# Optimization experiments

Measured on AMD Instinct MI355X. Metric: run time of the kernel, lower is better.

Reference implementation:

```python
import jax, jax.numpy as jnp
import numpy as np

N_NODES = 50000
N_EDGES = 200000
D = 384
R = 2  # num_relations


def setup_inputs() -> dict:
    key = jax.random.key(0)
    ks = jax.random.split(key, 16)
    inp = {
        "embeddings": jax.random.normal(ks[0], (N_NODES, D), dtype=jnp.float32),
        "edge_index": jax.random.randint(ks[1], (2, N_EDGES), 0, N_NODES, dtype=jnp.int64),
        "edge_type": jax.random.randint(ks[2], (N_EDGES,), 0, R, dtype=jnp.int64),
    }
    # RGCNConv params for 3 layers: per-relation weight, root weight, bias
    s = 1.0 / np.sqrt(D)
    for i, kk in zip((1, 2, 3), range(3)):
        inp[f"W{i}"] = jax.random.uniform(ks[3 + 3 * kk], (R, D, D), dtype=jnp.float32, minval=-s, maxval=s)
        inp[f"root{i}"] = jax.random.uniform(ks[4 + 3 * kk], (D, D), dtype=jnp.float32, minval=-s, maxval=s)
        inp[f"bias{i}"] = jnp.zeros((D,), dtype=jnp.float32)
    return inp


def _rgcn_conv(x, src, dst, edge_type, W, root, bias):
    # PyG RGCNConv with aggr='mean': for each relation, mean-aggregate neighbor
    # features over edges of that relation, then apply relation weight; plus
    # root transform and bias. We transform-then-aggregate (equivalent, linear).
    out = x @ root + bias
    for r in range(R):
        xr = x @ W[r]                                   # [N, D]
        mask = (edge_type == r).astype(x.dtype)         # [E]
        msg = xr[src] * mask[:, None]                   # [E, D] gather
        s = jax.ops.segment_sum(msg, dst, num_segments=N_NODES)    # [N, D]
        cnt = jax.ops.segment_sum(mask, dst, num_segments=N_NODES)  # [N]
        out = out + s / jnp.maximum(cnt, 1.0)[:, None]  # mean (0 if no edges)
    return out


def reference(embeddings, edge_index, edge_type, W1, root1, bias1, W2, root2, bias2, W3, root3, bias3):
    src, dst = edge_index[0], edge_index[1]
    x = jax.nn.relu(_rgcn_conv(embeddings, src, dst, edge_type, W1, root1, bias1))
    # dropout is identity in eval mode
    x = jax.nn.relu(_rgcn_conv(x, src, dst, edge_type, W2, root2, bias2))
    x = _rgcn_conv(x, src, dst, edge_type, W3, root3, bias3)
    return x
```

## Files before the change

### kernel.cpp

```cpp
#include <hip/hip_runtime.h>
#include <hip/hip_bf16.h>


#define D 384
#define KC 1152
#define BM 128
#define BN 128
#define BK 32
#define NKT (KC / BK)
#define NTN (D / BN)

typedef __attribute__((ext_vector_type(8))) short short8;
typedef __attribute__((ext_vector_type(4))) float floatx4;
typedef unsigned int uint;
typedef unsigned short ushort;

#define BAR() asm volatile("s_barrier" ::: "memory")
#define WAIT_VM4() asm volatile("s_waitcnt vmcnt(4)" ::: "memory")
#define WAIT_VM0() asm volatile("s_waitcnt vmcnt(0)" ::: "memory")

__device__ __forceinline__ void load_lds16(const void* g, void* l) {
    __builtin_amdgcn_global_load_lds(
        (const __attribute__((address_space(1))) void*)g,
        (__attribute__((address_space(3))) void*)l, 16, 0, 0);
}

__device__ __forceinline__ ushort f2bf(float x) {
    __hip_bfloat16 h = __float2bfloat16(x);
    return *reinterpret_cast<ushort*>(&h);
}

__device__ __forceinline__ uint pack2(float a, float b) {
    return (uint)f2bf(a) | ((uint)f2bf(b) << 16);
}

__device__ __forceinline__ float bflo(uint u) { return __uint_as_float(u << 16); }
__device__ __forceinline__ float bfhi(uint u) { return __uint_as_float(u & 0xffff0000u); }

__device__ __forceinline__ void stage_rows(const ushort* __restrict__ g,
                                           size_t stride, int koff,
                                           ushort* l, int grow0, int rmax,
                                           int tid)
{
#pragma unroll
    for (int j = 0; j < 2; ++j) {
        const int ch = j * 256 + tid;
        const int row = ch >> 2;
        const int cs = ch & 3;
        const int gc = cs ^ ((row >> 1) & 3);
        const int gr = min(grow0 + row, rmax);
        load_lds16(g + (size_t)gr * stride + koff + gc * 8, l + (size_t)ch * 8);
    }
}

__global__ __launch_bounds__(256, 3) void gemm_fused(
    const ushort* __restrict__ X, const ushort* __restrict__ AG,
    const ushort* __restrict__ BT, const float* __restrict__ bias,
    ushort* __restrict__ Xn, float* __restrict__ outf,
    int M, int nwg, int relu)
{
    __shared__ alignas(16) ushort As[3][BM * BK];
    __shared__ alignas(16) ushort Bs[3][BN * BK];

    const int o = blockIdx.x;
    const int xcd = o & 7, lid = o >> 3;
    const int q = nwg >> 3, r = nwg & 7;
    const int wg = (xcd < r ? xcd * (q + 1) : r * (q + 1) + (xcd - r) * q) + lid;
    const int bnt = wg % NTN, bmt = wg / NTN;
    const int bm = bmt * BM, bn = bnt * BN;

    const int tid = threadIdx.x;
    const int wave = tid >> 6, lane = tid & 63;
    const int wm = wave >> 1;
    const int wn = wave & 1;
    const int l15 = lane & 15, k8 = lane >> 4;

    floatx4 acc[4][4] = {};

    auto stage_a = [&](int kt, ushort* dst) {
        if (kt < 12) stage_rows(X, 384, kt * BK, dst, bm, M - 1, tid);
        else         stage_rows(AG, 768, (kt - 12) * BK, dst, bm, M - 1, tid);
    };

    stage_a(0, As[0]);
    stage_rows(BT, KC, 0, Bs[0], bn, D - 1, tid);
    stage_a(1, As[1]);
    stage_rows(BT, KC, BK, Bs[1], bn, D - 1, tid);
    WAIT_VM4();
    BAR();

    for (int j = 0; j < NKT; ++j) {
        const ushort* Ab = As[j % 3];
        const ushort* Bb = Bs[j % 3];

        short8 af[4], bf[4];
#pragma unroll
        for (int nf = 0; nf < 4; ++nf) {
            const int rr = wn * 64 + nf * 16 + l15;
            af[nf] = *(const short8*)(Bb + rr * BK + ((k8 ^ ((rr >> 1) & 3)) << 3));
        }
#pragma unroll
        for (int mf = 0; mf < 4; ++mf) {
            const int rr = wm * 64 + mf * 16 + l15;
            bf[mf] = *(const short8*)(Ab + rr * BK + ((k8 ^ ((rr >> 1) & 3)) << 3));
        }

        const int js = j + 2;
        if (js < NKT) {
            stage_a(js, As[js % 3]);
            stage_rows(BT, KC, js * BK, Bs[js % 3], bn, D - 1, tid);
        }

        __builtin_amdgcn_s_setprio(1);
#pragma unroll
        for (int nf = 0; nf < 4; ++nf)
#pragma unroll
            for (int mf = 0; mf < 4; ++mf)
                acc[nf][mf] = __builtin_amdgcn_mfma_f32_16x16x32_bf16(
                    af[nf], bf[mf], acc[nf][mf], 0, 0, 0);
        __builtin_amdgcn_s_setprio(0);

        if (j <= NKT - 3)      { WAIT_VM4(); }
        else if (j == NKT - 2) { WAIT_VM0(); }
        BAR();
    }

    const int node0 = bm + wm * 64 + l15;
    const int colg = bn + wn * 64 + k8 * 4;
    float4 bv[4];
#pragma unroll
    for (int nf = 0; nf < 4; ++nf)
        bv[nf] = *(const float4*)(bias + colg + nf * 16);

#pragma unroll
    for (int mf = 0; mf < 4; ++mf) {
        const int node = node0 + mf * 16;
        if (node < M) {
            float v[4][4];
#pragma unroll
            for (int nf = 0; nf < 4; ++nf) {
                v[nf][0] = acc[nf][mf][0] + bv[nf].x;
                v[nf][1] = acc[nf][mf][1] + bv[nf].y;
                v[nf][2] = acc[nf][mf][2] + bv[nf].z;
                v[nf][3] = acc[nf][mf][3] + bv[nf].w;
                if (relu) {
#pragma unroll
                    for (int t = 0; t < 4; ++t) v[nf][t] = fmaxf(v[nf][t], 0.f);
                }
            }
            if (Xn) {
                uint2* rowp = (uint2*)(Xn + (size_t)node * D + colg);
#pragma unroll
                for (int nf = 0; nf < 4; ++nf) {
                    uint2 o2;
                    o2.x = pack2(v[nf][0], v[nf][1]);
                    o2.y = pack2(v[nf][2], v[nf][3]);
                    rowp[nf * 4] = o2;
                }
            } else {
                float4* rowp = (float4*)(outf + (size_t)node * D + colg);
#pragma unroll
                for (int nf = 0; nf < 4; ++nf)
                    rowp[nf * 4] = make_float4(v[nf][0], v[nf][1],
                                               v[nf][2], v[nf][3]);
            }
        }
    }
}


__global__ __launch_bounds__(256) void count_edges(
    const int* __restrict__ dst, const int* __restrict__ et,
    int* __restrict__ cntI, int E, int M)
{
    const int e = blockIdx.x * blockDim.x + threadIdx.x;
    if (e < E) atomicAdd(&cntI[(size_t)et[e] * M + dst[e]], 1);
}

__global__ __launch_bounds__(1024) void scan_local(
    int* __restrict__ hist, int* __restrict__ offs,
    int* __restrict__ bsums, float* __restrict__ invc, int n)
{
    __shared__ int tmp[1024];
    const int tid = threadIdx.x;
    const int i = blockIdx.x * 1024 + tid;
    const int v = (i < n) ? hist[i] : 0;
    if (i < n) {
        invc[i] = 1.0f / (float)max(v, 1);
        hist[i] = 0;
    }
    tmp[tid] = v;
    __syncthreads();
#pragma unroll
    for (int off = 1; off < 1024; off <<= 1) {
        const int add = (tid >= off) ? tmp[tid - off] : 0;
        __syncthreads();
        tmp[tid] += add;
        __syncthreads();
    }
    if (i < n) offs[i] = tmp[tid] - v;
    if (tid == 1023) bsums[blockIdx.x] = tmp[1023];
}

__global__ __launch_bounds__(1024) void scan_bsums(
    int* __restrict__ bsums, int* __restrict__ total_out, int nb)
{
    __shared__ int tmp[1024];
    const int tid = threadIdx.x;
    const int v = (tid < nb) ? bsums[tid] : 0;
    tmp[tid] = v;
    __syncthreads();
#pragma unroll
    for (int off = 1; off < 1024; off <<= 1) {
        const int add = (tid >= off) ? tmp[tid - off] : 0;
        __syncthreads();
        tmp[tid] += add;
        __syncthreads();
    }
    if (tid < nb) bsums[tid] = tmp[tid] - v;
    if (tid == 1023) *total_out = tmp[1023];
}

__global__ __launch_bounds__(1024) void scan_add(
    int* __restrict__ offs, const int* __restrict__ bsums, int n)
{
    const int i = blockIdx.x * 1024 + threadIdx.x;
    if (i < n) offs[i] += bsums[blockIdx.x];
}

__global__ __launch_bounds__(256) void fill_sorted(
    const int* __restrict__ src, const int* __restrict__ dst,
    const int* __restrict__ et, const int* __restrict__ offs,
    int* __restrict__ cursor, int* __restrict__ sorted, int E, int M)
{
    const int e = blockIdx.x * blockDim.x + threadIdx.x;
    if (e < E) {
        const int key = et[e] * M + dst[e];
        const int pos = offs[key] + atomicAdd(&cursor[key], 1);
        sorted[pos] = src[e];
    }
}

__global__ __launch_bounds__(256) void build_bt(
    const float* __restrict__ root1, const float* __restrict__ W1,
    const float* __restrict__ root2, const float* __restrict__ W2,
    const float* __restrict__ root3, const float* __restrict__ W3,
    ushort* __restrict__ BT)
{
    __shared__ float tile[32][33];
    const int l = blockIdx.z;
    const float* root = (l == 0) ? root1 : (l == 1) ? root2 : root3;
    const float* W    = (l == 0) ? W1    : (l == 1) ? W2    : W3;
    const int k0 = blockIdx.x * 32;
    const int n0 = blockIdx.y * 32;
    const int tx = threadIdx.x & 31;
    const int ty = threadIdx.x >> 5;
    const float* srcm;
    int koff;
    if (k0 < D)          { srcm = root;      koff = 0; }
    else if (k0 < 2 * D) { srcm = W;         koff = D; }
    else                 { srcm = W + D * D; koff = 2 * D; }
#pragma unroll
    for (int i = 0; i < 4; ++i) {
        const int k = k0 - koff + ty + i * 8;
        tile[ty + i * 8][tx] = srcm[(size_t)k * D + n0 + tx];
    }
    __syncthreads();
    ushort* dst = BT + (size_t)l * D * KC;
#pragma unroll
    for (int i = 0; i < 4; ++i) {
        const int nn = n0 + ty + i * 8;
        const int kk = k0 + tx;
        dst[(size_t)nn * KC + kk] = f2bf(tile[tx][ty + i * 8]);
    }
}

__global__ __launch_bounds__(256) void cast_f32_to_bf16(
    const float* __restrict__ x, ushort* __restrict__ y, int n4)
{
    const int i = blockIdx.x * blockDim.x + threadIdx.x;
    if (i < n4) {
        const float4 v = ((const float4*)x)[i];
        uint2 o;
        o.x = pack2(v.x, v.y);
        o.y = pack2(v.z, v.w);
        ((uint2*)y)[i] = o;
    }
}

__global__ __launch_bounds__(256) void aggregate_rel(
    const ushort* __restrict__ X, const int* __restrict__ sorted,
    const int* __restrict__ offs, const float* __restrict__ invc,
    ushort* __restrict__ AG, int M)
{
    const int wave = threadIdx.x >> 6;
    const int lane = threadIdx.x & 63;
    const int key = blockIdx.x * 4 + wave;
    if (key >= 2 * M) return;
    const int r = (key >= M) ? 1 : 0;
    const int d = key - (r ? M : 0);

    const int beg = offs[key], end = offs[key + 1];
    const bool act = lane < 48;
    float g0 = 0.f, g1 = 0.f, g2 = 0.f, g3 = 0.f,
          g4 = 0.f, g5 = 0.f, g6 = 0.f, g7 = 0.f;

    for (int base = beg; base < end; base += 64) {
        const int cnt = min(end - base, 64);
        const int idx = (lane < cnt) ? sorted[base + lane] : 0;
        int e = 0;
        for (; e + 2 <= cnt; e += 2) {
            const int s0 = __shfl(idx, e);
            const int s1 = __shfl(idx, e + 1);
            if (act) {
                const uint4 a = ((const uint4*)(X + (size_t)s0 * D))[lane];
                const uint4 b = ((const uint4*)(X + (size_t)s1 * D))[lane];
                g0 += bflo(a.x) + bflo(b.x);  g1 += bfhi(a.x) + bfhi(b.x);
                g2 += bflo(a.y) + bflo(b.y);  g3 += bfhi(a.y) + bfhi(b.y);
                g4 += bflo(a.z) + bflo(b.z);  g5 += bfhi(a.z) + bfhi(b.z);
                g6 += bflo(a.w) + bflo(b.w);  g7 += bfhi(a.w) + bfhi(b.w);
            }
        }
        if (e < cnt) {
            const int s0 = __shfl(idx, e);
            if (act) {
                const uint4 a = ((const uint4*)(X + (size_t)s0 * D))[lane];
                g0 += bflo(a.x);  g1 += bfhi(a.x);
                g2 += bflo(a.y);  g3 += bfhi(a.y);
                g4 += bflo(a.z);  g5 += bfhi(a.z);
                g6 += bflo(a.w);  g7 += bfhi(a.w);
            }
        }
    }

    if (act) {
        const float ic = invc[key];
        uint4 o;
        o.x = pack2(ic * g0, ic * g1);
        o.y = pack2(ic * g2, ic * g3);
        o.z = pack2(ic * g4, ic * g5);
        o.w = pack2(ic * g6, ic * g7);
        ((uint4*)(AG + (size_t)d * (2 * D) + r * D))[lane] = o;
    }
}

extern "C" void kernel_launch(void* const* d_in, const int* in_sizes, int n_in,
                              void* d_out, int out_size, void* d_ws, size_t ws_size,
                              hipStream_t stream)
{
    const float* emb   = (const float*)d_in[0];
    const int*   eidx  = (const int*)d_in[1];
    const int*   et    = (const int*)d_in[2];
    const float* W1    = (const float*)d_in[3];
    const float* root1 = (const float*)d_in[4];
    const float* bias1 = (const float*)d_in[5];
    const float* W2    = (const float*)d_in[6];
    const float* root2 = (const float*)d_in[7];
    const float* bias2 = (const float*)d_in[8];
    const float* W3    = (const float*)d_in[9];
    const float* root3 = (const float*)d_in[10];
    const float* bias3 = (const float*)d_in[11];

    float* out = (float*)d_out;
    const int M = in_sizes[0] / D;
    const int E = in_sizes[1] / 2;
    const int* src  = eidx;
    const int* dstv = eidx + E;

    const int n = 2 * M;
    const int nb = (n + 1023) / 1024;

    char* w = (char*)d_ws;
    ushort* Xa  = (ushort*)w;         w += (size_t)M * D * 2;
    ushort* Xb2 = (ushort*)w;         w += (size_t)M * D * 2;
    ushort* AG  = (ushort*)w;         w += (size_t)M * 2 * D * 2;
    ushort* BT  = (ushort*)w;         w += (size_t)3 * D * KC * 2;
    float* invcnt = (float*)w;        w += (size_t)n * 4;
    int* cntI = (int*)w;              w += (size_t)n * 4;
    int* offs = (int*)w;              w += ((size_t)n + 1) * 4;
    int* sorted = (int*)w;            w += (size_t)E * 4;
    int* bsums = (int*)w;

    hipMemsetAsync(cntI, 0, (size_t)n * sizeof(int), stream);
    count_edges<<<(E + 255) / 256, 256, 0, stream>>>(dstv, et, cntI, E, M);
    scan_local<<<nb, 1024, 0, stream>>>(cntI, offs, bsums, invcnt, n);
    scan_bsums<<<1, 1024, 0, stream>>>(bsums, offs + n, nb);
    scan_add<<<nb, 1024, 0, stream>>>(offs, bsums, n);
    fill_sorted<<<(E + 255) / 256, 256, 0, stream>>>(src, dstv, et, offs, cntI, sorted, E, M);

    build_bt<<<dim3(KC / 32, D / 32, 3), 256, 0, stream>>>(root1, W1, root2, W2, root3, W3, BT);
    cast_f32_to_bf16<<<(M * D / 4 + 255) / 256, 256, 0, stream>>>(emb, Xa, M * D / 4);

    const int Mtiles = (M + BM - 1) / BM;
    const int nwg = Mtiles * NTN;
    const int agg_blocks = (2 * M + 3) / 4;

    aggregate_rel<<<agg_blocks, 256, 0, stream>>>(Xa, sorted, offs, invcnt, AG, M);
    gemm_fused<<<nwg, 256, 0, stream>>>(Xa, AG, BT, bias1, Xb2, nullptr, M, nwg, 1);
    aggregate_rel<<<agg_blocks, 256, 0, stream>>>(Xb2, sorted, offs, invcnt, AG, M);
    gemm_fused<<<nwg, 256, 0, stream>>>(Xb2, AG, BT + (size_t)D * KC, bias2, Xa, nullptr, M, nwg, 1);
    aggregate_rel<<<agg_blocks, 256, 0, stream>>>(Xa, sorted, offs, invcnt, AG, M);
    gemm_fused<<<nwg, 256, 0, stream>>>(Xa, AG, BT + (size_t)2 * D * KC, bias3, nullptr, out, M, nwg, 0);
}
```

Baseline: 475.1 us.

## Load weight fragments directly to registers from a pre-swizzled fragment layout

The weight-prep kernel now writes the bf16 transposed weights in an MFMA-fragment-ordered layout, so each lane's 16-byte fragment is contiguous. The GEMM drops the B LDS staging buffers and loads B fragments straight from global memory into a rotating triple set of registers two k-steps ahead, with the loop unrolled by three to keep register indexing static. This frees LDS and removes LDS traffic for B, which may allow more occupancy. In exchange it raises register pressure and depends on global/L2 latency for B being hidden by the prefetch depth.

New measurement: 626.5 us. +31.9%, slower.

```diff
diff --git a/kernel.cpp b/kernel.cpp
--- a/kernel.cpp
+++ b/kernel.cpp
@@ -16,7 +16,7 @@
 typedef unsigned short ushort;
 
 #define BAR() asm volatile("s_barrier" ::: "memory")
-#define WAIT_VM4() asm volatile("s_waitcnt vmcnt(4)" ::: "memory")
+#define WAIT_VM6() asm volatile("s_waitcnt vmcnt(6)" ::: "memory")
 #define WAIT_VM0() asm volatile("s_waitcnt vmcnt(0)" ::: "memory")
 
 __device__ __forceinline__ void load_lds16(const void* g, void* l) {
@@ -55,12 +55,11 @@
 
 __global__ __launch_bounds__(256, 3) void gemm_fused(
     const ushort* __restrict__ X, const ushort* __restrict__ AG,
-    const ushort* __restrict__ BT, const float* __restrict__ bias,
+    const ushort* __restrict__ BTt, const float* __restrict__ bias,
     ushort* __restrict__ Xn, float* __restrict__ outf,
     int M, int nwg, int relu)
 {
     __shared__ alignas(16) ushort As[3][BM * BK];
-    __shared__ alignas(16) ushort Bs[3][BN * BK];
 
     const int o = blockIdx.x;
     const int xcd = o & 7, lid = o >> 3;
@@ -82,48 +81,58 @@
         else         stage_rows(AG, 768, (kt - 12) * BK, dst, bm, M - 1, tid);
     };
 
-    stage_a(0, As[0]);
-    stage_rows(BT, KC, 0, Bs[0], bn, D - 1, tid);
-    stage_a(1, As[1]);
-    stage_rows(BT, KC, BK, Bs[1], bn, D - 1, tid);
-    WAIT_VM4();
-    BAR();
-
-    for (int j = 0; j < NKT; ++j) {
-        const ushort* Ab = As[j % 3];
-        const ushort* Bb = Bs[j % 3];
-
-        short8 af[4], bf[4];
-#pragma unroll
-        for (int nf = 0; nf < 4; ++nf) {
-            const int rr = wn * 64 + nf * 16 + l15;
-            af[nf] = *(const short8*)(Bb + rr * BK + ((k8 ^ ((rr >> 1) & 3)) << 3));
+    auto bload = [&](int kt, short8* wf) {
+#pragma unroll
+        for (int nf2 = 0; nf2 < 4; ++nf2) {
+            const int rg = (bn >> 4) + wn * 4 + nf2;
+            wf[nf2] = *(const short8*)(
+                BTt + (((size_t)rg * 144 + kt * 4 + k8) * 16 + l15) * 8);
         }
+    };
+    auto aread = [&](const ushort* Ab, short8* nfr) {
 #pragma unroll
         for (int mf = 0; mf < 4; ++mf) {
             const int rr = wm * 64 + mf * 16 + l15;
-            bf[mf] = *(const short8*)(Ab + rr * BK + ((k8 ^ ((rr >> 1) & 3)) << 3));
+            nfr[mf] = *(const short8*)(Ab + rr * BK + ((k8 ^ ((rr >> 1) & 3)) << 3));
         }
-
-        const int js = j + 2;
-        if (js < NKT) {
-            stage_a(js, As[js % 3]);
-            stage_rows(BT, KC, js * BK, Bs[js % 3], bn, D - 1, tid);
-        }
-
-        __builtin_amdgcn_s_setprio(1);
-#pragma unroll
-        for (int nf = 0; nf < 4; ++nf)
-#pragma unroll
-            for (int mf = 0; mf < 4; ++mf)
-                acc[nf][mf] = __builtin_amdgcn_mfma_f32_16x16x32_bf16(
-                    af[nf], bf[mf], acc[nf][mf], 0, 0, 0);
-        __builtin_amdgcn_s_setprio(0);
-
-        if (j <= NKT - 3)      { WAIT_VM4(); }
-        else if (j == NKT - 2) { WAIT_VM0(); }
-        BAR();
-    }
+    };
+
+    short8 wf0[4], wf1[4], wf2[4];
+
+    stage_a(0, As[0]);
+    bload(0, wf0);
+    stage_a(1, As[1]);
+    bload(1, wf1);
+    WAIT_VM0();
+    BAR();
+
+#define GSEG(t, SLOT, WFCUR, WFNXT2)                                         \
+    {                                                                        \
+        short8 nfr[4];                                                       \
+        aread(As[SLOT], nfr);                                                \
+        if ((t) + 2 < NKT) {                                                 \
+            bload((t) + 2, WFNXT2);                                          \
+            stage_a((t) + 2, As[((SLOT) + 2) % 3]);                          \
+        }                                                                    \
+        __builtin_amdgcn_s_setprio(1);                                       \
+        _Pragma("unroll")                                                    \
+        for (int nf2 = 0; nf2 < 4; ++nf2)                                    \
+            _Pragma("unroll")                                                \
+            for (int mf = 0; mf < 4; ++mf)                                   \
+                acc[nf2][mf] = __builtin_amdgcn_mfma_f32_16x16x32_bf16(      \
+                    WFCUR[nf2], nfr[mf], acc[nf2][mf], 0, 0, 0);             \
+        __builtin_amdgcn_s_setprio(0);                                       \
+        if ((t) <= NKT - 3)      { WAIT_VM6(); }                             \
+        else if ((t) == NKT - 2) { WAIT_VM0(); }                             \
+        BAR();                                                               \
+    }
+
+    for (int t3 = 0; t3 < NKT; t3 += 3) {
+        GSEG(t3 + 0, 0, wf0, wf2)
+        GSEG(t3 + 1, 1, wf1, wf0)
+        GSEG(t3 + 2, 2, wf2, wf1)
+    }
+#undef GSEG
 
     const int node0 = bm + wm * 64 + l15;
     const int colg = bn + wn * 64 + k8 * 4;
@@ -271,7 +280,8 @@
     for (int i = 0; i < 4; ++i) {
         const int nn = n0 + ty + i * 8;
         const int kk = k0 + tx;
-        dst[(size_t)nn * KC + kk] = f2bf(tile[tx][ty + i * 8]);
+        dst[(((size_t)(nn >> 4) * 144 + (kk >> 3)) * 16 + (nn & 15)) * 8 + (kk & 7)]
+            = f2bf(tile[tx][ty + i * 8]);
     }
 }
 
```
